# Kernel tuning notes

Measured on AMD Instinct MI355X. Metric: run time of the kernel, lower is better.

The kernel has to match this reference:

```python
import jax, jax.numpy as jnp
import numpy as np

T, B, H, L = 64, 128, 256, 2  # steps/stack_size, batch, hidden, layers


def setup_inputs() -> dict:
    key = jax.random.key(0)
    ks = jax.random.split(key, 6)
    s = 1.0 / np.sqrt(H)
    x = jax.random.normal(ks[0], (T, B, H), dtype=jnp.float32)
    ops = jax.random.randint(ks[1], (T, B), 0, 2, dtype=jnp.int32)  # push=1, hold=0
    W_ih = jax.random.uniform(ks[2], (L, 4 * H, H), jnp.float32, -s, s)
    W_hh = jax.random.uniform(ks[3], (L, 4 * H, H), jnp.float32, -s, s)
    b_ih = jax.random.uniform(ks[4], (L, 4 * H), jnp.float32, -s, s)
    b_hh = jax.random.uniform(ks[5], (L, 4 * H), jnp.float32, -s, s)
    return {"x": x, "ops": ops, "W_ih": W_ih, "W_hh": W_hh, "b_ih": b_ih, "b_hh": b_hh}


def reference(x, ops, W_ih, W_hh, b_ih, b_hh):
    T_, B_, H_ = x.shape
    L_ = W_ih.shape[0]
    bidx = jnp.arange(B_)

    def cell(xt, h_prev, c_prev):
        # multi-layer LSTM cell; layer l>0 takes layer l-1 hidden as input (dropout=0)
        inp = xt
        hs, cs = [], []
        for l in range(L_):
            gates = inp @ W_ih[l].T + b_ih[l] + h_prev[..., l] @ W_hh[l].T + b_hh[l]
            i, f, g, o = jnp.split(gates, 4, axis=-1)
            c = jax.nn.sigmoid(f) * c_prev[..., l] + jax.nn.sigmoid(i) * jnp.tanh(g)
            h = jax.nn.sigmoid(o) * jnp.tanh(c)
            hs.append(h)
            cs.append(c)
            inp = h
        return jnp.stack(hs, axis=-1), jnp.stack(cs, axis=-1)  # (B, H, L)

    def step(carry, xt_op):
        hstack, cstack, pos = carry  # stacks: (T+1, B, H, L), pos: (B,)
        xt, opt = xt_op
        h_prev = hstack[pos, bidx]  # gather top-of-stack, (B, H, L)
        c_prev = cstack[pos, bidx]
        nh, nc = cell(xt, h_prev, c_prev)
        # hold_or_push writes at pos+1 for every batch element, then pos += op
        hstack = hstack.at[pos + 1, bidx].set(nh)
        cstack = cstack.at[pos + 1, bidx].set(nc)
        pos = pos + opt
        return (hstack, cstack, pos), nh[..., -1]  # last-layer hidden output

    hs0 = jnp.zeros((T_ + 1, B_, H_, L_), dtype=x.dtype)
    cs0 = jnp.zeros((T_ + 1, B_, H_, L_), dtype=x.dtype)
    pos0 = jnp.zeros((B_,), dtype=jnp.int32)
    _, outs = jax.lax.scan(step, (hs0, cs0, pos0), (x, ops))
    return outs  # (T, B, H)
```

## Files before the change

kernel.cpp:

```cpp
#include <hip/hip_runtime.h>
#include <hip/hip_fp16.h>
#include <cstddef>

#define TT 64
#define BB 128
#define HH 256
#define G4 1024
#define BLK 256
#define NBG 16
#define NHG 16

__device__ __forceinline__ float sigf(float x) { return 1.0f / (1.0f + expf(-x)); }

typedef _Float16 h2v __attribute__((ext_vector_type(2)));

__device__ __forceinline__ float dot2acc(unsigned w, unsigned h, float acc) {
#if __has_builtin(__builtin_amdgcn_fdot2)
  return __builtin_amdgcn_fdot2(__builtin_bit_cast(h2v, w),
                                __builtin_bit_cast(h2v, h), acc, false);
#else
  __half2 wv = *(__half2*)&w, hv = *(__half2*)&h;
  float2 wf = __half22float2(wv), hf = __half22float2(hv);
  return fmaf(wf.x, hf.x, fmaf(wf.y, hf.y, acc));
#endif
}

__device__ __forceinline__ unsigned packh2(float e, float o) {
  return (unsigned)__half_as_ushort(__float2half(e)) |
         ((unsigned)__half_as_ushort(__float2half(o)) << 16);
}

__device__ __forceinline__ int hsw8(int b, int k2) {
  return b * 144 + k2 + ((k2 >> 5) << 2);
}

__global__ void __launch_bounds__(BLK, 2)
seq10(const float* __restrict__ x,
      const int* __restrict__ ops,
      const float* __restrict__ W_ih,
      const float* __restrict__ W_hh,
      const float* __restrict__ b_ih,
      const float* __restrict__ b_hh,
      float* __restrict__ ws,
      float* __restrict__ out) {
  const int role = blockIdx.x >> 8;
  const int bh = blockIdx.x & 255;
  const int bg = bh & 15;
  const int hg = bh >> 4;
  const int tid = threadIdx.x;
  const int kq = tid & 7;
  const int c2 = tid >> 3;

  __shared__ __align__(16) float smem[6272];
  __shared__ int opsA[TT * 8];

  unsigned long long* __restrict__ Hx0 = (unsigned long long*)ws;
  unsigned long long* __restrict__ Hx1 = Hx0 + (size_t)TT * NBG * 1024;

  for (int i = tid; i < TT * 8; i += BLK)
    opsA[i] = ops[(i >> 3) * BB + bg * 8 + (i & 7)];

  const int pb = tid >> 5;
  const int pk2 = (tid & 31) * 4;

  if (role == 0) {
    float* xbufs = smem;
    unsigned* hp0 = (unsigned*)(smem + 4608);
    float* gatA = smem + 5760;

    unsigned wr0[32];
    float wx0[64];
    float bias0r[2];
#pragma unroll
    for (int j = 0; j < 2; ++j) {
      const int lc = c2 * 2 + j;
      const int g = ((lc >> 4) << 8) + hg * 16 + (lc & 15);
      const float* ph = W_hh + (size_t)g * HH + kq * 32;
      const float* pw = W_ih + (size_t)g * HH + kq * 32;
#pragma unroll
      for (int i = 0; i < 16; ++i)
        wr0[j * 16 + i] = packh2(ph[2 * i], ph[2 * i + 1]);
#pragma unroll
      for (int i = 0; i < 32; ++i) wx0[j * 32 + i] = pw[i];
      bias0r[j] = b_ih[g] + b_hh[g];
    }
    for (int i = tid; i < 8 * 144; i += BLK) hp0[i] = 0u;
    {
      const float4* xsrc = (const float4*)(x + (size_t)bg * 8 * HH);
#pragma unroll
      for (int i2 = 0; i2 < 2; ++i2) {
        const int f4 = tid + i2 * 256;
        const float4 v = xsrc[f4];
        const int b = f4 >> 6, k4 = f4 & 63;
        *(float4*)&xbufs[b * 288 + (k4 >> 3) * 36 + (k4 & 7) * 4] = v;
      }
    }
    __syncthreads();

    float xf[8][2];
#pragma unroll
    for (int b = 0; b < 8; ++b) {
      const float* xb = &xbufs[b * 288 + kq * 36];
      float s0 = 0.f, s1 = 0.f;
#pragma unroll
      for (int k = 0; k < 32; ++k) {
        s0 = fmaf(wx0[k], xb[k], s0);
        s1 = fmaf(wx0[32 + k], xb[k], s1);
      }
#pragma unroll
      for (int m = 1; m <= 4; m <<= 1) {
        s0 += __shfl_xor(s0, m, 64);
        s1 += __shfl_xor(s1, m, 64);
      }
      xf[b][0] = s0; xf[b][1] = s1;
    }
    float a0r[8][2] = {};
    float cp0 = 0.f;

    for (int t = 0; t < TT; ++t) {
      if (t > 0 && opsA[(t - 1) * 8 + pb]) {
        const unsigned long long* sp = Hx0 + ((size_t)(t - 1) * NBG + bg) * 1024;
        const unsigned tag = (unsigned)t;
        unsigned long long v[4];
        bool d[4] = {false, false, false, false};
        int spins = 0;
        for (;;) {
#pragma unroll
          for (int i = 0; i < 4; ++i)
            if (!d[i]) v[i] = __hip_atomic_load(sp + tid * 4 + i, __ATOMIC_RELAXED,
                                                __HIP_MEMORY_SCOPE_AGENT);
          bool all = true;
#pragma unroll
          for (int i = 0; i < 4; ++i) { d[i] = d[i] || ((unsigned)v[i] == tag); all &= d[i]; }
          if (all) break;
          if (++spins > (1 << 18)) break;
          if (spins > 2) __builtin_amdgcn_s_sleep(1);
        }
        *(uint4*)&hp0[hsw8(pb, pk2)] =
            make_uint4((unsigned)(v[0] >> 32), (unsigned)(v[1] >> 32),
                       (unsigned)(v[2] >> 32), (unsigned)(v[3] >> 32));
      }
      __syncthreads();

#pragma unroll
      for (int b = 0; b < 8; ++b) {
        if (t > 0 && opsA[(t - 1) * 8 + b]) {
          const unsigned* hb = &hp0[b * 144 + kq * 16 + ((kq >> 1) << 2)];
          const uint4 x0 = *(const uint4*)(hb + 0);
          const uint4 x1 = *(const uint4*)(hb + 4);
          const uint4 x2 = *(const uint4*)(hb + 8);
          const uint4 x3 = *(const uint4*)(hb + 12);
          const unsigned hh[16] = {x0.x, x0.y, x0.z, x0.w, x1.x, x1.y, x1.z, x1.w,
                                   x2.x, x2.y, x2.z, x2.w, x3.x, x3.y, x3.z, x3.w};
          float s0 = 0.f, s1 = 0.f;
#pragma unroll
          for (int i = 0; i < 16; ++i) {
            s0 = dot2acc(wr0[i], hh[i], s0);
            s1 = dot2acc(wr0[16 + i], hh[i], s1);
          }
#pragma unroll
          for (int m = 1; m <= 4; m <<= 1) {
            s0 += __shfl_xor(s0, m, 64);
            s1 += __shfl_xor(s1, m, 64);
          }
          a0r[b][0] = s0; a0r[b][1] = s1;
        }
      }
      if (kq == 0) {
#pragma unroll
        for (int b = 0; b < 8; ++b)
          *(float2*)&gatA[b * 64 + c2 * 2] =
              make_float2(xf[b][0] + a0r[b][0] + bias0r[0],
                          xf[b][1] + a0r[b][1] + bias0r[1]);
      }
      __syncthreads();

      if (tid < 128) {
        const int b = tid >> 4, r = tid & 15;
        const float* gt = &gatA[b * 64];
        const float ig = gt[r], fg = gt[16 + r], gg = gt[32 + r], og = gt[48 + r];
        const float c = sigf(fg) * cp0 + sigf(ig) * tanhf(gg);
        const float h = sigf(og) * tanhf(c);
        if (opsA[t * 8 + b]) cp0 = c;
        const float ho = __shfl_xor(h, 1, 64);
        if (!(r & 1)) {
          const unsigned long long vv =
              (unsigned long long)(unsigned)(t + 1) |
              ((unsigned long long)packh2(h, ho) << 32);
          __hip_atomic_store(
              Hx0 + ((size_t)t * NBG + bg) * 1024 + b * 128 + hg * 8 + (r >> 1),
              vv, __ATOMIC_RELAXED, __HIP_MEMORY_SCOPE_AGENT);
        }
      }
      if (t < TT - 1) {
        float* xd = &xbufs[((t + 1) & 1) * 2304];
        const float4* xsrc = (const float4*)(x + ((size_t)(t + 1) * BB + bg * 8) * HH);
#pragma unroll
        for (int i2 = 0; i2 < 2; ++i2) {
          const int f4 = tid + i2 * 256;
          const float4 v = xsrc[f4];
          const int b = f4 >> 6, k4 = f4 & 63;
          *(float4*)&xd[b * 288 + (k4 >> 3) * 36 + (k4 & 7) * 4] = v;
        }
        __syncthreads();
#pragma unroll
        for (int b = 0; b < 8; ++b) {
          const float* xb = &xd[b * 288 + kq * 36];
          float s0 = 0.f, s1 = 0.f;
#pragma unroll
          for (int k = 0; k < 32; ++k) {
            s0 = fmaf(wx0[k], xb[k], s0);
            s1 = fmaf(wx0[32 + k], xb[k], s1);
          }
#pragma unroll
          for (int m = 1; m <= 4; m <<= 1) {
            s0 += __shfl_xor(s0, m, 64);
            s1 += __shfl_xor(s1, m, 64);
          }
          xf[b][0] = s0; xf[b][1] = s1;
        }
      }
    }
  } else {
    unsigned* h0c = (unsigned*)smem;
    unsigned* hp1 = (unsigned*)(smem + 1152);
    float* gatB = smem + 2304;

    unsigned wr1[32], wr2[32];
    float bias1r[2];
#pragma unroll
    for (int j = 0; j < 2; ++j) {
      const int lc = c2 * 2 + j;
      const int g = ((lc >> 4) << 8) + hg * 16 + (lc & 15);
      const float* p1 = W_ih + (size_t)G4 * HH + (size_t)g * HH + kq * 32;
      const float* p2 = W_hh + (size_t)G4 * HH + (size_t)g * HH + kq * 32;
#pragma unroll
      for (int i = 0; i < 16; ++i) {
        wr1[j * 16 + i] = packh2(p1[2 * i], p1[2 * i + 1]);
        wr2[j * 16 + i] = packh2(p2[2 * i], p2[2 * i + 1]);
      }
      bias1r[j] = b_ih[G4 + g] + b_hh[G4 + g];
    }
    for (int i = tid; i < 8 * 144; i += BLK) hp1[i] = 0u;
    float a1q[8][2] = {};
    float cp1 = 0.f;
    __syncthreads();

    for (int t = 0; t < TT; ++t) {
      {
        const unsigned long long* sp0 = Hx0 + ((size_t)t * NBG + bg) * 1024;
        const unsigned long long* sp1 =
            Hx1 + ((size_t)(t > 0 ? t - 1 : 0) * NBG + bg) * 1024;
        const unsigned tagA = (unsigned)(t + 1), tagB = (unsigned)t;
        const bool need1 = (t > 0) && (opsA[(t - 1) * 8 + pb] != 0);
        unsigned long long v[4], w[4];
        bool dv[4] = {false, false, false, false};
        bool dw[4] = {!need1, !need1, !need1, !need1};
        int spins = 0;
        for (;;) {
#pragma unroll
          for (int i = 0; i < 4; ++i) {
            if (!dv[i]) v[i] = __hip_atomic_load(sp0 + tid * 4 + i, __ATOMIC_RELAXED,
                                                 __HIP_MEMORY_SCOPE_AGENT);
            if (!dw[i]) w[i] = __hip_atomic_load(sp1 + tid * 4 + i, __ATOMIC_RELAXED,
                                                 __HIP_MEMORY_SCOPE_AGENT);
          }
          bool all = true;
#pragma unroll
          for (int i = 0; i < 4; ++i) {
            dv[i] = dv[i] || ((unsigned)v[i] == tagA);
            dw[i] = dw[i] || ((unsigned)w[i] == tagB);
            all = all && dv[i] && dw[i];
          }
          if (all) break;
          if (++spins > (1 << 18)) break;
          if (spins > 2) __builtin_amdgcn_s_sleep(1);
        }
        *(uint4*)&h0c[hsw8(pb, pk2)] =
            make_uint4((unsigned)(v[0] >> 32), (unsigned)(v[1] >> 32),
                       (unsigned)(v[2] >> 32), (unsigned)(v[3] >> 32));
        if (need1)
          *(uint4*)&hp1[hsw8(pb, pk2)] =
              make_uint4((unsigned)(w[0] >> 32), (unsigned)(w[1] >> 32),
                         (unsigned)(w[2] >> 32), (unsigned)(w[3] >> 32));
      }
      __syncthreads();

      float fr[8][2];
#pragma unroll
      for (int b = 0; b < 8; ++b) {
        const unsigned* cb = &h0c[b * 144 + kq * 16 + ((kq >> 1) << 2)];
        const uint4 c0 = *(const uint4*)(cb + 0);
        const uint4 c1 = *(const uint4*)(cb + 4);
        const uint4 c2v = *(const uint4*)(cb + 8);
        const uint4 c3 = *(const uint4*)(cb + 12);
        const unsigned hc[16] = {c0.x, c0.y, c0.z, c0.w, c1.x, c1.y, c1.z, c1.w,
                                 c2v.x, c2v.y, c2v.z, c2v.w, c3.x, c3.y, c3.z, c3.w};
        float s0 = 0.f, s1 = 0.f;
#pragma unroll
        for (int i = 0; i < 16; ++i) {
          s0 = dot2acc(wr1[i], hc[i], s0);
          s1 = dot2acc(wr1[16 + i], hc[i], s1);
        }
        if (t > 0 && opsA[(t - 1) * 8 + b]) {
          const unsigned* qb = &hp1[b * 144 + kq * 16 + ((kq >> 1) << 2)];
          const uint4 q0 = *(const uint4*)(qb + 0);
          const uint4 q1 = *(const uint4*)(qb + 4);
          const uint4 q2 = *(const uint4*)(qb + 8);
          const uint4 q3 = *(const uint4*)(qb + 12);
          const unsigned hq[16] = {q0.x, q0.y, q0.z, q0.w, q1.x, q1.y, q1.z, q1.w,
                                   q2.x, q2.y, q2.z, q2.w, q3.x, q3.y, q3.z, q3.w};
          float t0 = 0.f, t1 = 0.f;
#pragma unroll
          for (int i = 0; i < 16; ++i) {
            t0 = dot2acc(wr2[i], hq[i], t0);
            t1 = dot2acc(wr2[16 + i], hq[i], t1);
          }
#pragma unroll
          for (int m = 1; m <= 4; m <<= 1) {
            t0 += __shfl_xor(t0, m, 64);
            t1 += __shfl_xor(t1, m, 64);
          }
          a1q[b][0] = t0; a1q[b][1] = t1;
        }
#pragma unroll
        for (int m = 1; m <= 4; m <<= 1) {
          s0 += __shfl_xor(s0, m, 64);
          s1 += __shfl_xor(s1, m, 64);
        }
        fr[b][0] = s0; fr[b][1] = s1;
      }
      if (kq == 0) {
#pragma unroll
        for (int b = 0; b < 8; ++b)
          *(float2*)&gatB[b * 64 + c2 * 2] =
              make_float2(fr[b][0] + a1q[b][0] + bias1r[0],
                          fr[b][1] + a1q[b][1] + bias1r[1]);
      }
      __syncthreads();

      if (tid < 128) {
        const int b = tid >> 4, r = tid & 15;
        const float* gt = &gatB[b * 64];
        const float ig = gt[r], fg = gt[16 + r], gg = gt[32 + r], og = gt[48 + r];
        const float c = sigf(fg) * cp1 + sigf(ig) * tanhf(gg);
        const float h = sigf(og) * tanhf(c);
        const int op = opsA[t * 8 + b];
        if (op) cp1 = c;
        out[((size_t)t * BB + bg * 8 + b) * HH + hg * 16 + r] = h;
        const float ho = __shfl_xor(h, 1, 64);
        if (op && !(r & 1)) {
          const unsigned long long vv =
              (unsigned long long)(unsigned)(t + 1) |
              ((unsigned long long)packh2(h, ho) << 32);
          __hip_atomic_store(
              Hx1 + ((size_t)t * NBG + bg) * 1024 + b * 128 + hg * 8 + (r >> 1),
              vv, __ATOMIC_RELAXED, __HIP_MEMORY_SCOPE_AGENT);
        }
      }
    }
  }
}

extern "C" void kernel_launch(void* const* d_in, const int* in_sizes, int n_in,
                              void* d_out, int out_size, void* d_ws, size_t ws_size,
                              hipStream_t stream) {
  const float* x    = (const float*)d_in[0];
  const int*   ops  = (const int*)d_in[1];
  const float* W_ih = (const float*)d_in[2];
  const float* W_hh = (const float*)d_in[3];
  const float* b_ih = (const float*)d_in[4];
  const float* b_hh = (const float*)d_in[5];
  float* out = (float*)d_out;
  float* ws  = (float*)d_ws;

  seq10<<<512, BLK, 0, stream>>>(x, ops, W_ih, W_hh, b_ih, b_hh, ws, out);
}
```

Before: 467.1 us.

## Merge layer roles into one skewed pipeline with precomputed input projections

Replaces the two-role design (separate layer-0 and layer-1 blocks) with 256 blocks that each compute layer 0 at step t and layer 1 at step t-1 in one skewed loop. A single spin-wait then covers both exchanges. The layer-0 input projection for all timesteps is precomputed up front into workspace, taking it off the recurrent critical path. The hidden-state exchange buffers become a 4-deep ring instead of a per-timestep array. This cuts the number of barriers and cross-block waits per step, at the cost of more registers per thread (three weight sets), lower occupancy, and ring-reuse hazards if blocks drift apart.

After: 695.0 us. 48.8% more time.

```diff
diff --git a/kernel.cpp b/kernel.cpp
--- a/kernel.cpp
+++ b/kernel.cpp
@@ -8,7 +8,11 @@
 #define G4 1024
 #define BLK 256
 #define NBG 16
-#define NHG 16
+#define RING 4
+
+#define OFF_XG  0u
+#define OFF_HX0 8388608u
+#define OFF_HX1 8519680u
 
 __device__ __forceinline__ float sigf(float x) { return 1.0f / (1.0f + expf(-x)); }
 
@@ -34,8 +38,8 @@
   return b * 144 + k2 + ((k2 >> 5) << 2);
 }
 
-__global__ void __launch_bounds__(BLK, 2)
-seq10(const float* __restrict__ x,
+__global__ void __launch_bounds__(BLK, 1)
+seq11(const float* __restrict__ x,
       const int* __restrict__ ops,
       const float* __restrict__ W_ih,
       const float* __restrict__ W_hh,
@@ -43,108 +47,161 @@
       const float* __restrict__ b_hh,
       float* __restrict__ ws,
       float* __restrict__ out) {
-  const int role = blockIdx.x >> 8;
-  const int bh = blockIdx.x & 255;
-  const int bg = bh & 15;
-  const int hg = bh >> 4;
+  const int bg = blockIdx.x & 15;
+  const int hg = blockIdx.x >> 4;
   const int tid = threadIdx.x;
   const int kq = tid & 7;
   const int c2 = tid >> 3;
 
-  __shared__ __align__(16) float smem[6272];
+  __shared__ __align__(16) unsigned smh[3 * 1152];
+  __shared__ __align__(16) float gatA[8 * 68];
+  __shared__ __align__(16) float gatB[8 * 68];
   __shared__ int opsA[TT * 8];
 
-  unsigned long long* __restrict__ Hx0 = (unsigned long long*)ws;
-  unsigned long long* __restrict__ Hx1 = Hx0 + (size_t)TT * NBG * 1024;
+  unsigned* h0c = smh;
+  unsigned* hp0 = smh + 1152;
+  unsigned* hp1 = smh + 2304;
 
   for (int i = tid; i < TT * 8; i += BLK)
     opsA[i] = ops[(i >> 3) * BB + bg * 8 + (i & 7)];
 
-  const int pb = tid >> 5;
-  const int pk2 = (tid & 31) * 4;
-
-  if (role == 0) {
-    float* xbufs = smem;
-    unsigned* hp0 = (unsigned*)(smem + 4608);
-    float* gatA = smem + 5760;
-
-    unsigned wr0[32];
+  float* __restrict__ Xg = ws + OFF_XG + (size_t)(bg * 16 + hg) * 32768;
+  unsigned long long* __restrict__ Hx0 = (unsigned long long*)(ws + OFF_HX0);
+  unsigned long long* __restrict__ Hx1 = (unsigned long long*)(ws + OFF_HX1);
+
+  {
     float wx0[64];
-    float bias0r[2];
+    float pb0[2];
 #pragma unroll
     for (int j = 0; j < 2; ++j) {
       const int lc = c2 * 2 + j;
       const int g = ((lc >> 4) << 8) + hg * 16 + (lc & 15);
-      const float* ph = W_hh + (size_t)g * HH + kq * 32;
       const float* pw = W_ih + (size_t)g * HH + kq * 32;
 #pragma unroll
-      for (int i = 0; i < 16; ++i)
-        wr0[j * 16 + i] = packh2(ph[2 * i], ph[2 * i + 1]);
-#pragma unroll
       for (int i = 0; i < 32; ++i) wx0[j * 32 + i] = pw[i];
-      bias0r[j] = b_ih[g] + b_hh[g];
-    }
-    for (int i = tid; i < 8 * 144; i += BLK) hp0[i] = 0u;
-    {
-      const float4* xsrc = (const float4*)(x + (size_t)bg * 8 * HH);
-#pragma unroll
-      for (int i2 = 0; i2 < 2; ++i2) {
-        const int f4 = tid + i2 * 256;
-        const float4 v = xsrc[f4];
-        const int b = f4 >> 6, k4 = f4 & 63;
-        *(float4*)&xbufs[b * 288 + (k4 >> 3) * 36 + (k4 & 7) * 4] = v;
-      }
+      pb0[j] = b_ih[g] + b_hh[g];
+    }
+    float* xs = (float*)smh;
+    for (int t = 0; t < TT; ++t) {
+      const float4* xsrc = (const float4*)(x + ((size_t)t * BB + bg * 8) * HH);
+      const float4 va = xsrc[tid];
+      const float4 vb = xsrc[tid + 256];
+      __syncthreads();
+      {
+        const int b0_ = tid >> 6, k40 = tid & 63;
+        *(float4*)&xs[b0_ * 288 + (k40 >> 3) * 36 + (k40 & 7) * 4] = va;
+        const int f4 = tid + 256;
+        const int b1_ = f4 >> 6, k41 = f4 & 63;
+        *(float4*)&xs[b1_ * 288 + (k41 >> 3) * 36 + (k41 & 7) * 4] = vb;
+      }
+      __syncthreads();
+#pragma unroll
+      for (int b = 0; b < 8; ++b) {
+        const float* xb = &xs[b * 288 + kq * 36];
+        float s0 = 0.f, s1 = 0.f;
+#pragma unroll
+        for (int k = 0; k < 32; k += 4) {
+          const float4 xv = *(const float4*)&xb[k];
+          s0 = fmaf(wx0[k], xv.x, s0);
+          s0 = fmaf(wx0[k + 1], xv.y, s0);
+          s0 = fmaf(wx0[k + 2], xv.z, s0);
+          s0 = fmaf(wx0[k + 3], xv.w, s0);
+          s1 = fmaf(wx0[32 + k], xv.x, s1);
+          s1 = fmaf(wx0[32 + k + 1], xv.y, s1);
+          s1 = fmaf(wx0[32 + k + 2], xv.z, s1);
+          s1 = fmaf(wx0[32 + k + 3], xv.w, s1);
+        }
+#pragma unroll
+        for (int m = 1; m <= 4; m <<= 1) {
+          s0 += __shfl_xor(s0, m, 64);
+          s1 += __shfl_xor(s1, m, 64);
+        }
+        if (kq == 0)
+          *(float2*)&Xg[(size_t)t * 512 + b * 64 + c2 * 2] =
+              make_float2(s0 + pb0[0], s1 + pb0[1]);
+      }
+    }
+  }
+
+  unsigned wr0[32], wr1[32], wr2[32];
+  float bias1r[2];
+#pragma unroll
+  for (int j = 0; j < 2; ++j) {
+    const int lc = c2 * 2 + j;
+    const int g = ((lc >> 4) << 8) + hg * 16 + (lc & 15);
+    const float* p0 = W_hh + (size_t)g * HH + kq * 32;
+    const float* p1 = W_ih + (size_t)G4 * HH + (size_t)g * HH + kq * 32;
+    const float* p2 = W_hh + (size_t)G4 * HH + (size_t)g * HH + kq * 32;
+#pragma unroll
+    for (int i = 0; i < 16; ++i) {
+      wr0[j * 16 + i] = packh2(p0[2 * i], p0[2 * i + 1]);
+      wr1[j * 16 + i] = packh2(p1[2 * i], p1[2 * i + 1]);
+      wr2[j * 16 + i] = packh2(p2[2 * i], p2[2 * i + 1]);
+    }
+    bias1r[j] = b_ih[G4 + g] + b_hh[G4 + g];
+  }
+
+  const int pb = tid >> 5;
+  const int pk2 = (tid & 31) * 4;
+  float a0r[8][2] = {};
+  float a1q[8][2] = {};
+  float cp0 = 0.f, cp1 = 0.f;
+
+  for (int t = 0; t <= TT; ++t) {
+    float xg0 = 0.f, xg1 = 0.f, xg2 = 0.f, xg3 = 0.f;
+    if (t < TT && tid < 128) {
+      const int b = tid >> 4, r = tid & 15;
+      const float* xp = &Xg[(size_t)t * 512 + b * 64 + r];
+      xg0 = xp[0]; xg1 = xp[16]; xg2 = xp[32]; xg3 = xp[48];
+    }
+    if (t >= 1) {
+      const unsigned long long* sp0 =
+          Hx0 + ((size_t)((t - 1) & (RING - 1)) * NBG + bg) * 1024;
+      const unsigned tag0 = (unsigned)t;
+      const bool need1 = (t >= 2) && (opsA[(t - 2) * 8 + pb] != 0);
+      const unsigned long long* sp1 =
+          Hx1 + ((size_t)((t >= 2 ? t - 2 : 0) & (RING - 1)) * NBG + bg) * 1024;
+      const unsigned tag1 = (unsigned)(t - 1);
+      unsigned long long v[4], w[4] = {0, 0, 0, 0};
+      bool dv[4] = {false, false, false, false};
+      bool dw[4] = {!need1, !need1, !need1, !need1};
+      int spins = 0;
+      for (;;) {
+#pragma unroll
+        for (int i = 0; i < 4; ++i) {
+          if (!dv[i]) v[i] = __hip_atomic_load(sp0 + tid * 4 + i, __ATOMIC_RELAXED,
+                                               __HIP_MEMORY_SCOPE_AGENT);
+          if (!dw[i]) w[i] = __hip_atomic_load(sp1 + tid * 4 + i, __ATOMIC_RELAXED,
+                                               __HIP_MEMORY_SCOPE_AGENT);
+        }
+        bool all = true;
+#pragma unroll
+        for (int i = 0; i < 4; ++i) {
+          dv[i] = dv[i] || ((unsigned)v[i] == tag0);
+          dw[i] = dw[i] || ((unsigned)w[i] == tag1);
+          all = all && dv[i] && dw[i];
+        }
+        if (all) break;
+        if (++spins > (1 << 18)) break;
+        if (spins > 2) __builtin_amdgcn_s_sleep(1);
+      }
+      const int sw = hsw8(pb, pk2);
+      const uint4 pay =
+          make_uint4((unsigned)(v[0] >> 32), (unsigned)(v[1] >> 32),
+                     (unsigned)(v[2] >> 32), (unsigned)(v[3] >> 32));
+      *(uint4*)&h0c[sw] = pay;
+      if (opsA[(t - 1) * 8 + pb]) *(uint4*)&hp0[sw] = pay;
+      if (need1)
+        *(uint4*)&hp1[sw] =
+            make_uint4((unsigned)(w[0] >> 32), (unsigned)(w[1] >> 32),
+                       (unsigned)(w[2] >> 32), (unsigned)(w[3] >> 32));
     }
     __syncthreads();
 
-    float xf[8][2];
-#pragma unroll
-    for (int b = 0; b < 8; ++b) {
-      const float* xb = &xbufs[b * 288 + kq * 36];
-      float s0 = 0.f, s1 = 0.f;
-#pragma unroll
-      for (int k = 0; k < 32; ++k) {
-        s0 = fmaf(wx0[k], xb[k], s0);
-        s1 = fmaf(wx0[32 + k], xb[k], s1);
-      }
-#pragma unroll
-      for (int m = 1; m <= 4; m <<= 1) {
-        s0 += __shfl_xor(s0, m, 64);
-        s1 += __shfl_xor(s1, m, 64);
-      }
-      xf[b][0] = s0; xf[b][1] = s1;
-    }
-    float a0r[8][2] = {};
-    float cp0 = 0.f;
-
-    for (int t = 0; t < TT; ++t) {
-      if (t > 0 && opsA[(t - 1) * 8 + pb]) {
-        const unsigned long long* sp = Hx0 + ((size_t)(t - 1) * NBG + bg) * 1024;
-        const unsigned tag = (unsigned)t;
-        unsigned long long v[4];
-        bool d[4] = {false, false, false, false};
-        int spins = 0;
-        for (;;) {
-#pragma unroll
-          for (int i = 0; i < 4; ++i)
-            if (!d[i]) v[i] = __hip_atomic_load(sp + tid * 4 + i, __ATOMIC_RELAXED,
-                                                __HIP_MEMORY_SCOPE_AGENT);
-          bool all = true;
-#pragma unroll
-          for (int i = 0; i < 4; ++i) { d[i] = d[i] || ((unsigned)v[i] == tag); all &= d[i]; }
-          if (all) break;
-          if (++spins > (1 << 18)) break;
-          if (spins > 2) __builtin_amdgcn_s_sleep(1);
-        }
-        *(uint4*)&hp0[hsw8(pb, pk2)] =
-            make_uint4((unsigned)(v[0] >> 32), (unsigned)(v[1] >> 32),
-                       (unsigned)(v[2] >> 32), (unsigned)(v[3] >> 32));
-      }
-      __syncthreads();
-
+    if (t >= 1 && t < TT) {
 #pragma unroll
       for (int b = 0; b < 8; ++b) {
-        if (t > 0 && opsA[(t - 1) * 8 + b]) {
+        if (opsA[(t - 1) * 8 + b]) {
           const unsigned* hb = &hp0[b * 144 + kq * 16 + ((kq >> 1) << 2)];
           const uint4 x0 = *(const uint4*)(hb + 0);
           const uint4 x1 = *(const uint4*)(hb + 4);
@@ -166,19 +223,68 @@
           a0r[b][0] = s0; a0r[b][1] = s1;
         }
       }
-      if (kq == 0) {
-#pragma unroll
-        for (int b = 0; b < 8; ++b)
-          *(float2*)&gatA[b * 64 + c2 * 2] =
-              make_float2(xf[b][0] + a0r[b][0] + bias0r[0],
-                          xf[b][1] + a0r[b][1] + bias0r[1]);
-      }
-      __syncthreads();
-
-      if (tid < 128) {
+    }
+    if (t >= 1) {
+#pragma unroll
+      for (int b = 0; b < 8; ++b) {
+        const unsigned* cb = &h0c[b * 144 + kq * 16 + ((kq >> 1) << 2)];
+        const uint4 c0 = *(const uint4*)(cb + 0);
+        const uint4 c1 = *(const uint4*)(cb + 4);
+        const uint4 c2v = *(const uint4*)(cb + 8);
+        const uint4 c3 = *(const uint4*)(cb + 12);
+        const unsigned hc[16] = {c0.x, c0.y, c0.z, c0.w, c1.x, c1.y, c1.z, c1.w,
+                                 c2v.x, c2v.y, c2v.z, c2v.w, c3.x, c3.y, c3.z, c3.w};
+        float s0 = 0.f, s1 = 0.f;
+#pragma unroll
+        for (int i = 0; i < 16; ++i) {
+          s0 = dot2acc(wr1[i], hc[i], s0);
+          s1 = dot2acc(wr1[16 + i], hc[i], s1);
+        }
+        if (t >= 2 && opsA[(t - 2) * 8 + b]) {
+          const unsigned* qb = &hp1[b * 144 + kq * 16 + ((kq >> 1) << 2)];
+          const uint4 q0 = *(const uint4*)(qb + 0);
+          const uint4 q1 = *(const uint4*)(qb + 4);
+          const uint4 q2 = *(const uint4*)(qb + 8);
+          const uint4 q3 = *(const uint4*)(qb + 12);
+          const unsigned hq[16] = {q0.x, q0.y, q0.z, q0.w, q1.x, q1.y, q1.z, q1.w,
+                                   q2.x, q2.y, q2.z, q2.w, q3.x, q3.y, q3.z, q3.w};
+          float t0 = 0.f, t1 = 0.f;
+#pragma unroll
+          for (int i = 0; i < 16; ++i) {
+            t0 = dot2acc(wr2[i], hq[i], t0);
+            t1 = dot2acc(wr2[16 + i], hq[i], t1);
+          }
+#pragma unroll
+          for (int m = 1; m <= 4; m <<= 1) {
+            t0 += __shfl_xor(t0, m, 64);
+            t1 += __shfl_xor(t1, m, 64);
+          }
+          a1q[b][0] = t0; a1q[b][1] = t1;
+        }
+#pragma unroll
+        for (int m = 1; m <= 4; m <<= 1) {
+          s0 += __shfl_xor(s0, m, 64);
+          s1 += __shfl_xor(s1, m, 64);
+        }
+        if (kq == 0)
+          *(float2*)&gatB[b * 68 + c2 * 2] =
+              make_float2(s0 + a1q[b][0] + bias1r[0],
+                          s1 + a1q[b][1] + bias1r[1]);
+      }
+    }
+    if (t < TT && kq == 0) {
+#pragma unroll
+      for (int b = 0; b < 8; ++b)
+        *(float2*)&gatA[b * 68 + c2 * 2] = make_float2(a0r[b][0], a0r[b][1]);
+    }
+    __syncthreads();
+
+    if (tid < 128) {
+      if (t < TT) {
         const int b = tid >> 4, r = tid & 15;
-        const float* gt = &gatA[b * 64];
-        const float ig = gt[r], fg = gt[16 + r], gg = gt[32 + r], og = gt[48 + r];
+        const float* gt = &gatA[b * 68];
+        const float ig = gt[r] + xg0,      fg = gt[16 + r] + xg1;
+        const float gg = gt[32 + r] + xg2, og = gt[48 + r] + xg3;
         const float c = sigf(fg) * cp0 + sigf(ig) * tanhf(gg);
         const float h = sigf(og) * tanhf(c);
         if (opsA[t * 8 + b]) cp0 = c;
@@ -188,175 +294,31 @@
               (unsigned long long)(unsigned)(t + 1) |
               ((unsigned long long)packh2(h, ho) << 32);
           __hip_atomic_store(
-              Hx0 + ((size_t)t * NBG + bg) * 1024 + b * 128 + hg * 8 + (r >> 1),
+              Hx0 + ((size_t)(t & (RING - 1)) * NBG + bg) * 1024 +
+                  b * 128 + hg * 8 + (r >> 1),
               vv, __ATOMIC_RELAXED, __HIP_MEMORY_SCOPE_AGENT);
         }
       }
-      if (t < TT - 1) {
-        float* xd = &xbufs[((t + 1) & 1) * 2304];
-        const float4* xsrc = (const float4*)(x + ((size_t)(t + 1) * BB + bg * 8) * HH);
-#pragma unroll
-        for (int i2 = 0; i2 < 2; ++i2) {
-          const int f4 = tid + i2 * 256;
-          const float4 v = xsrc[f4];
-          const int b = f4 >> 6, k4 = f4 & 63;
-          *(float4*)&xd[b * 288 + (k4 >> 3) * 36 + (k4 & 7) * 4] = v;
-        }
-        __syncthreads();
-#pragma unroll
-        for (int b = 0; b < 8; ++b) {
-          const float* xb = &xd[b * 288 + kq * 36];
-          float s0 = 0.f, s1 = 0.f;
-#pragma unroll
-          for (int k = 0; k < 32; ++k) {
-            s0 = fmaf(wx0[k], xb[k], s0);
-            s1 = fmaf(wx0[32 + k], xb[k], s1);
-          }
-#pragma unroll
-          for (int m = 1; m <= 4; m <<= 1) {
-            s0 += __shfl_xor(s0, m, 64);
-            s1 += __shfl_xor(s1, m, 64);
-          }
-          xf[b][0] = s0; xf[b][1] = s1;
-        }
-      }
-    }
-  } else {
-    unsigned* h0c = (unsigned*)smem;
-    unsigned* hp1 = (unsigned*)(smem + 1152);
-    float* gatB = smem + 2304;
-
-    unsigned wr1[32], wr2[32];
-    float bias1r[2];
-#pragma unroll
-    for (int j = 0; j < 2; ++j) {
-      const int lc = c2 * 2 + j;
-      const int g = ((lc >> 4) << 8) + hg * 16 + (lc & 15);
-      const float* p1 = W_ih + (size_t)G4 * HH + (size_t)g * HH + kq * 32;
-      const float* p2 = W_hh + (size_t)G4 * HH + (size_t)g * HH + kq * 32;
-#pragma unroll
-      for (int i = 0; i < 16; ++i) {
-        wr1[j * 16 + i] = packh2(p1[2 * i], p1[2 * i + 1]);
-        wr2[j * 16 + i] = packh2(p2[2 * i], p2[2 * i + 1]);
-      }
-      bias1r[j] = b_ih[G4 + g] + b_hh[G4 + g];
-    }
-    for (int i = tid; i < 8 * 144; i += BLK) hp1[i] = 0u;
-    float a1q[8][2] = {};
-    float cp1 = 0.f;
-    __syncthreads();
-
-    for (int t = 0; t < TT; ++t) {
-      {
-        const unsigned long long* sp0 = Hx0 + ((size_t)t * NBG + bg) * 1024;
-        const unsigned long long* sp1 =
-            Hx1 + ((size_t)(t > 0 ? t - 1 : 0) * NBG + bg) * 1024;
-        const unsigned tagA = (unsigned)(t + 1), tagB = (unsigned)t;
-        const bool need1 = (t > 0) && (opsA[(t - 1) * 8 + pb] != 0);
-        unsigned long long v[4], w[4];
-        bool dv[4] = {false, false, false, false};
-        bool dw[4] = {!need1, !need1, !need1, !need1};
-        int spins = 0;
-        for (;;) {
-#pragma unroll
-          for (int i = 0; i < 4; ++i) {
-            if (!dv[i]) v[i] = __hip_atomic_load(sp0 + tid * 4 + i, __ATOMIC_RELAXED,
-                                                 __HIP_MEMORY_SCOPE_AGENT);
-            if (!dw[i]) w[i] = __hip_atomic_load(sp1 + tid * 4 + i, __ATOMIC_RELAXED,
-                                                 __HIP_MEMORY_SCOPE_AGENT);
-          }
-          bool all = true;
-#pragma unroll
-          for (int i = 0; i < 4; ++i) {
-            dv[i] = dv[i] || ((unsigned)v[i] == tagA);
-            dw[i] = dw[i] || ((unsigned)w[i] == tagB);
-            all = all && dv[i] && dw[i];
-          }
-          if (all) break;
-          if (++spins > (1 << 18)) break;
-          if (spins > 2) __builtin_amdgcn_s_sleep(1);
-        }
-        *(uint4*)&h0c[hsw8(pb, pk2)] =
-            make_uint4((unsigned)(v[0] >> 32), (unsigned)(v[1] >> 32),
-                       (unsigned)(v[2] >> 32), (unsigned)(v[3] >> 32));
-        if (need1)
-          *(uint4*)&hp1[hsw8(pb, pk2)] =
-              make_uint4((unsigned)(w[0] >> 32), (unsigned)(w[1] >> 32),
-                         (unsigned)(w[2] >> 32), (unsigned)(w[3] >> 32));
-      }
-      __syncthreads();
-
-      float fr[8][2];
-#pragma unroll
-      for (int b = 0; b < 8; ++b) {
-        const unsigned* cb = &h0c[b * 144 + kq * 16 + ((kq >> 1) << 2)];
-        const uint4 c0 = *(const uint4*)(cb + 0);
-        const uint4 c1 = *(const uint4*)(cb + 4);
-        const uint4 c2v = *(const uint4*)(cb + 8);
-        const uint4 c3 = *(const uint4*)(cb + 12);
-        const unsigned hc[16] = {c0.x, c0.y, c0.z, c0.w, c1.x, c1.y, c1.z, c1.w,
-                                 c2v.x, c2v.y, c2v.z, c2v.w, c3.x, c3.y, c3.z, c3.w};
-        float s0 = 0.f, s1 = 0.f;
-#pragma unroll
-        for (int i = 0; i < 16; ++i) {
-          s0 = dot2acc(wr1[i], hc[i], s0);
-          s1 = dot2acc(wr1[16 + i], hc[i], s1);
-        }
-        if (t > 0 && opsA[(t - 1) * 8 + b]) {
-          const unsigned* qb = &hp1[b * 144 + kq * 16 + ((kq >> 1) << 2)];
-          const uint4 q0 = *(const uint4*)(qb + 0);
-          const uint4 q1 = *(const uint4*)(qb + 4);
-          const uint4 q2 = *(const uint4*)(qb + 8);
-          const uint4 q3 = *(const uint4*)(qb + 12);
-          const unsigned hq[16] = {q0.x, q0.y, q0.z, q0.w, q1.x, q1.y, q1.z, q1.w,
-                                   q2.x, q2.y, q2.z, q2.w, q3.x, q3.y, q3.z, q3.w};
-          float t0 = 0.f, t1 = 0.f;
-#pragma unroll
-          for (int i = 0; i < 16; ++i) {
-            t0 = dot2acc(wr2[i], hq[i], t0);
-            t1 = dot2acc(wr2[16 + i], hq[i], t1);
-          }
-#pragma unroll
-          for (int m = 1; m <= 4; m <<= 1) {
-            t0 += __shfl_xor(t0, m, 64);
-            t1 += __shfl_xor(t1, m, 64);
-          }
-          a1q[b][0] = t0; a1q[b][1] = t1;
-        }
-#pragma unroll
-        for (int m = 1; m <= 4; m <<= 1) {
-          s0 += __shfl_xor(s0, m, 64);
-          s1 += __shfl_xor(s1, m, 64);
-        }
-        fr[b][0] = s0; fr[b][1] = s1;
-      }
-      if (kq == 0) {
-#pragma unroll
-        for (int b = 0; b < 8; ++b)
-          *(float2*)&gatB[b * 64 + c2 * 2] =
-              make_float2(fr[b][0] + a1q[b][0] + bias1r[0],
-                          fr[b][1] + a1q[b][1] + bias1r[1]);
-      }
-      __syncthreads();
-
-      if (tid < 128) {
-        const int b = tid >> 4, r = tid & 15;
-        const float* gt = &gatB[b * 64];
-        const float ig = gt[r], fg = gt[16 + r], gg = gt[32 + r], og = gt[48 + r];
-        const float c = sigf(fg) * cp1 + sigf(ig) * tanhf(gg);
-        const float h = sigf(og) * tanhf(c);
-        const int op = opsA[t * 8 + b];
-        if (op) cp1 = c;
-        out[((size_t)t * BB + bg * 8 + b) * HH + hg * 16 + r] = h;
-        const float ho = __shfl_xor(h, 1, 64);
-        if (op && !(r & 1)) {
-          const unsigned long long vv =
-              (unsigned long long)(unsigned)(t + 1) |
-              ((unsigned long long)packh2(h, ho) << 32);
-          __hip_atomic_store(
-              Hx1 + ((size_t)t * NBG + bg) * 1024 + b * 128 + hg * 8 + (r >> 1),
-              vv, __ATOMIC_RELAXED, __HIP_MEMORY_SCOPE_AGENT);
-        }
+    } else if (t >= 1) {
+      const int s = t - 1;
+      const int b = (tid >> 4) & 7, r = tid & 15;
+      const float* gt = &gatB[b * 68];
+      const float ig = gt[r],      fg = gt[16 + r];
+      const float gg = gt[32 + r], og = gt[48 + r];
+      const float c = sigf(fg) * cp1 + sigf(ig) * tanhf(gg);
+      const float h = sigf(og) * tanhf(c);
+      const int op = opsA[s * 8 + b];
+      if (op) cp1 = c;
+      out[((size_t)s * BB + bg * 8 + b) * HH + hg * 16 + r] = h;
+      const float ho = __shfl_xor(h, 1, 64);
+      if (op && !(r & 1)) {
+        const unsigned long long vv =
+            (unsigned long long)(unsigned)(s + 1) |
+            ((unsigned long long)packh2(h, ho) << 32);
+        __hip_atomic_store(
+            Hx1 + ((size_t)(s & (RING - 1)) * NBG + bg) * 1024 +
+                b * 128 + hg * 8 + (r >> 1),
+            vv, __ATOMIC_RELAXED, __HIP_MEMORY_SCOPE_AGENT);
       }
     }
   }
@@ -374,5 +336,5 @@
   float* out = (float*)d_out;
   float* ws  = (float*)d_ws;
 
-  seq10<<<512, BLK, 0, stream>>>(x, ops, W_ih, W_hh, b_ih, b_hh, ws, out);
-}
+  seq11<<<256, BLK, 0, stream>>>(x, ops, W_ih, W_hh, b_ih, b_hh, ws, out);
+}
```
